# Kernel optimization log

Hardware: AMD Instinct MI355X
Metric: run time of the kernel (lower is better)

The kernel has to match this reference:

```python
import jax, jax.numpy as jnp
import numpy as np

B, T, C, HS = 8, 2048, 1024, 128


def setup_inputs() -> dict:
    key = jax.random.key(0)
    k1, k2, k3, k4 = jax.random.split(key, 4)
    return {
        "x": jax.random.normal(k1, (B, T, C), dtype=jnp.float32),
        "Wq": jax.random.normal(k2, (C, HS), dtype=jnp.float32) * (C ** -0.5),
        "Wk": jax.random.normal(k3, (C, HS), dtype=jnp.float32) * (C ** -0.5),
        "Wv": jax.random.normal(k4, (C, HS), dtype=jnp.float32) * (C ** -0.5),
    }


def _rope_tables(T, hs):
    # Matches get_rotary_embedding: d = hs//2, theta_i = 10000**(-2*(i-1)/d) for i in 0..d-1
    d = hs // 2
    i = jnp.arange(d, dtype=jnp.float32)
    theta = 10000.0 ** (-2.0 * (i - 1.0) / d)
    ang = jnp.arange(T, dtype=jnp.float32)[:, None] * theta[None, :]  # [T, d]
    return jnp.cos(ang), jnp.sin(ang)


def _rotate(t, c, s):
    # t: [B,T,hs]. Equivalent to t_m @ R_m with block-diag 2x2 rotations [[c,-s],[s,c]]:
    # out[2i] = e*c + o*s ; out[2i+1] = -e*s + o*c
    e, o = t[..., 0::2], t[..., 1::2]
    return jnp.stack([e * c + o * s, -e * s + o * c], axis=-1).reshape(t.shape)


def reference(x, Wq, Wk, Wv):
    Bx, Tx, Cx = x.shape
    hs = Wq.shape[1]
    c, s = _rope_tables(Tx, hs)
    q = _rotate(x @ Wq, c, s)  # [B,T,hs]
    k = _rotate(x @ Wk, c, s)
    v = x @ Wv
    scores = jnp.einsum("bqh,bkh->bqk", q, k) * (hs ** -0.5)  # [B,T,T]
    mask = jnp.tril(jnp.ones((Tx, Tx), dtype=bool))
    scores = jnp.where(mask, scores, -jnp.inf)
    A = jax.nn.softmax(scores, axis=-1)
    return jnp.einsum("bqk,bkh->bqh", A, v)
```

## Files before the change

### kernel.cpp

```cpp
#include <hip/hip_runtime.h>

typedef __bf16 bf16x8 __attribute__((ext_vector_type(8)));
typedef float f32x4 __attribute__((ext_vector_type(4)));

static __device__ __forceinline__ unsigned short f2bf(float f){
  unsigned int u = __builtin_bit_cast(unsigned int, f);
  u += 0x7FFFu + ((u >> 16) & 1u);
  return (unsigned short)(u >> 16);
}
static __device__ __forceinline__ float bf2f(unsigned short h){
  unsigned int u = ((unsigned int)h) << 16;
  return __builtin_bit_cast(float, u);
}

__global__ __launch_bounds__(256) void k_prepw(const float* __restrict__ Wq,
                                               const float* __restrict__ Wk,
                                               const float* __restrict__ Wv,
                                               unsigned short* __restrict__ Wtb){
  int idx = blockIdx.x * 256 + threadIdx.x;
  int m = idx >> 10;
  int k = idx & 1023;
  const float* W = (m < 128) ? Wq : ((m < 256) ? Wk : Wv);
  int n = m & 127;
  Wtb[idx] = f2bf(W[k * 128 + n]);
}

__global__ __launch_bounds__(512) void k_qkv(const float* __restrict__ x,
                                             const unsigned short* __restrict__ Wtb,
                                             unsigned short* __restrict__ Qr,
                                             unsigned short* __restrict__ Kr,
                                             unsigned short* __restrict__ Vt){
  __shared__ __align__(16) unsigned short lds[64 * 72 + 128 * 72];
  unsigned short* sA = lds;
  unsigned short* sB = lds + 64 * 72;

  int bid0 = blockIdx.x;
  int wg = (bid0 & 7) * 96 + (bid0 >> 3);
  int mblk = wg / 3;
  int nblk = wg - mblk * 3;

  int tid = threadIdx.x;
  int lane = tid & 63, wid = tid >> 6;
  int wm = wid >> 1, wn = wid & 1;
  int g = lane >> 4, lr = lane & 15;

  f32x4 acc[4] = {};
  const float* xbase = x + (size_t)(mblk * 64) * 1024;
  const unsigned short* wbase = Wtb + (size_t)(nblk * 128) * 1024;

  for (int k0 = 0; k0 < 1024; k0 += 64){
    __syncthreads();
#pragma unroll
    for (int p = 0; p < 2; p++){
      int idx = tid + p * 512;
      int r = idx >> 4, c4 = (idx & 15) * 4;
      float4 v = *reinterpret_cast<const float4*>(xbase + (size_t)r * 1024 + k0 + c4);
      uint2 pk;
      pk.x = ((unsigned int)f2bf(v.y) << 16) | f2bf(v.x);
      pk.y = ((unsigned int)f2bf(v.w) << 16) | f2bf(v.z);
      *reinterpret_cast<uint2*>(&sA[r * 72 + c4]) = pk;
    }
#pragma unroll
    for (int p = 0; p < 2; p++){
      int idx = tid + p * 512;
      int r = idx >> 3, c8 = (idx & 7) * 8;
      *reinterpret_cast<uint4*>(&sB[r * 72 + c8]) =
        *reinterpret_cast<const uint4*>(wbase + (size_t)r * 1024 + k0 + c8);
    }
    __syncthreads();

#pragma unroll
    for (int ks = 0; ks < 2; ks++){
      bf16x8 af = *reinterpret_cast<const bf16x8*>(&sA[(wm * 16 + lr) * 72 + ks * 32 + g * 8]);
      bf16x8 bfr[4];
#pragma unroll
      for (int n = 0; n < 4; n++)
        bfr[n] = *reinterpret_cast<const bf16x8*>(&sB[(wn * 64 + n * 16 + lr) * 72 + ks * 32 + g * 8]);
#pragma unroll
      for (int n = 0; n < 4; n++)
        acc[n] = __builtin_amdgcn_mfma_f32_16x16x32_bf16(af, bfr[n], acc[n], 0, 0, 0);
    }
  }
  __syncthreads();

  int row0 = mblk * 64;
  if (nblk < 2){
    unsigned short* sE = lds;
    float scale = nblk ? 1.0f : 0.12751744950370064f;
#pragma unroll
    for (int n = 0; n < 4; n++){
      int col = wn * 64 + n * 16 + lr;
      int i = col >> 1;
      float theta = exp2f(13.287712379549449f * (2.0f - 2.0f * (float)i) * 0.015625f);
      float sgn = (lr & 1) ? -1.0f : 1.0f;
#pragma unroll
      for (int r = 0; r < 4; r++){
        int tl = wm * 16 + g * 4 + r;
        int t = (row0 + tl) & 2047;
        float s, c;
        sincosf((float)t * theta, &s, &c);
        float v = acc[n][r];
        float partner = __shfl_xor(v, 1);
        float res = (v * c + partner * sgn * s) * scale;
        sE[tl * 136 + col] = f2bf(res);
      }
    }
    __syncthreads();
    unsigned short* dst = (nblk ? Kr : Qr) + (size_t)row0 * 128;
#pragma unroll
    for (int p = 0; p < 2; p++){
      int u = tid + p * 512;
      int tl = u >> 4, h0 = (u & 15) * 8;
      uint4 vv = *reinterpret_cast<const uint4*>(&sE[tl * 136 + h0]);
      *reinterpret_cast<uint4*>(dst + (size_t)tl * 128 + h0) = vv;
    }
  } else {
    unsigned short* sE = lds;
#pragma unroll
    for (int n = 0; n < 4; n++){
      int col = wn * 64 + n * 16 + lr;
#pragma unroll
      for (int r = 0; r < 4; r++){
        int tl = wm * 16 + g * 4 + r;
        sE[col * 72 + tl] = f2bf(acc[n][r]);
      }
    }
    __syncthreads();
    int b = row0 >> 11;
    int t0 = row0 & 2047;
#pragma unroll
    for (int p = 0; p < 2; p++){
      int u = tid + p * 512;
      int h = u >> 3, tc = (u & 7) * 8;
      uint4 vv = *reinterpret_cast<const uint4*>(&sE[h * 72 + tc]);
      *reinterpret_cast<uint4*>(Vt + ((size_t)(b * 128 + h)) * 2048 + t0 + tc) = vv;
    }
  }
}

__global__ __launch_bounds__(128) void k_attn_part(const unsigned short* __restrict__ Qr,
                                                   const unsigned short* __restrict__ Kr,
                                                   const unsigned short* __restrict__ Vt,
                                                   unsigned short* __restrict__ Opart,
                                                   float* __restrict__ ml){
  __shared__ __align__(16) unsigned short sK[32][136];
  __shared__ __align__(16) unsigned short sV[128][40];
  __shared__ __align__(16) unsigned short sP[2][16][40];

  int bid = blockIdx.x;
  int b = bid / 160;
  int rem = bid - b * 160;
  int qt, c;
  if (rem < 16)      { qt = rem;                    c = 0; }
  else if (rem < 48) { qt = 16 + ((rem - 16) >> 1); c = (rem - 16) & 1; }
  else if (rem < 96) { int r2 = rem - 48; int d = r2 / 3; qt = 32 + d; c = r2 - 3 * d; }
  else               { int r3 = rem - 96; qt = 48 + (r3 >> 2); c = r3 & 3; }

  int q_base = qt * 32;
  int kv_start = c * 512;
  int kv_end = min(kv_start + 512, q_base + 32);
  int niter = (kv_end - kv_start) >> 5;

  int tid = threadIdx.x, w = tid >> 6, lane = tid & 63;
  int g = lane >> 4, lr = lane & 15;

  int qrow = q_base + w * 16 + lr;
  const unsigned short* qptr = Qr + ((size_t)(b * 2048 + qrow)) * 128;
  bf16x8 qf[4];
#pragma unroll
  for (int hc = 0; hc < 4; hc++)
    qf[hc] = *reinterpret_cast<const bf16x8*>(qptr + hc * 32 + g * 8);

  f32x4 oacc[8] = {};
  float mrow = -1e30f, lrow = 0.0f;

  const unsigned short* Kb = Kr + (size_t)b * 2048 * 128;
  const unsigned short* Vb = Vt + (size_t)b * 128 * 2048;

  for (int it = 0; it < niter; it++){
    int kv0 = kv_start + it * 32;
    __syncthreads();
#pragma unroll
    for (int p = 0; p < 4; p++){
      int idx = tid + p * 128;
      int r = idx >> 4, c8 = (idx & 15) * 8;
      *reinterpret_cast<uint4*>(&sK[r][c8]) =
        *reinterpret_cast<const uint4*>(Kb + (size_t)(kv0 + r) * 128 + c8);
    }
#pragma unroll
    for (int p = 0; p < 4; p++){
      int idx = tid + p * 128;
      int h = idx >> 2, c8 = (idx & 3) * 8;
      *reinterpret_cast<uint4*>(&sV[h][c8]) =
        *reinterpret_cast<const uint4*>(Vb + (size_t)h * 2048 + kv0 + c8);
    }
    __syncthreads();

    f32x4 st[2];
#pragma unroll
    for (int ct = 0; ct < 2; ct++){
      f32x4 a = {0.f, 0.f, 0.f, 0.f};
#pragma unroll
      for (int hc = 0; hc < 4; hc++){
        bf16x8 kf = *reinterpret_cast<const bf16x8*>(&sK[ct * 16 + lr][hc * 32 + g * 8]);
        a = __builtin_amdgcn_mfma_f32_16x16x32_bf16(kf, qf[hc], a, 0, 0, 0);
      }
      st[ct] = a;
    }

    float mx = -1e30f;
#pragma unroll
    for (int ct = 0; ct < 2; ct++){
      int kvb = kv0 + ct * 16 + g * 4;
#pragma unroll
      for (int r = 0; r < 4; r++){
        float s = (kvb + r <= qrow) ? st[ct][r] : -1e30f;
        st[ct][r] = s;
        mx = fmaxf(mx, s);
      }
    }
    mx = fmaxf(mx, __shfl_xor(mx, 16));
    mx = fmaxf(mx, __shfl_xor(mx, 32));
    float m = fmaxf(mrow, mx);
    float alpha = exp2f(mrow - m);

    float rs = 0.0f;
#pragma unroll
    for (int ct = 0; ct < 2; ct++){
      float p0 = exp2f(st[ct][0] - m);
      float p1 = exp2f(st[ct][1] - m);
      float p2 = exp2f(st[ct][2] - m);
      float p3 = exp2f(st[ct][3] - m);
      rs += (p0 + p1) + (p2 + p3);
      uint2 pk;
      pk.x = ((unsigned int)f2bf(p1) << 16) | f2bf(p0);
      pk.y = ((unsigned int)f2bf(p3) << 16) | f2bf(p2);
      *reinterpret_cast<uint2*>(&sP[w][lr][ct * 16 + g * 4]) = pk;
    }
    rs += __shfl_xor(rs, 16);
    rs += __shfl_xor(rs, 32);
    lrow = lrow * alpha + rs;
    mrow = m;

    float af0 = __shfl(alpha, g * 4 + 0);
    float af1 = __shfl(alpha, g * 4 + 1);
    float af2 = __shfl(alpha, g * 4 + 2);
    float af3 = __shfl(alpha, g * 4 + 3);
#pragma unroll
    for (int ht = 0; ht < 8; ht++){
      oacc[ht][0] *= af0;
      oacc[ht][1] *= af1;
      oacc[ht][2] *= af2;
      oacc[ht][3] *= af3;
    }

    bf16x8 pa = *reinterpret_cast<const bf16x8*>(&sP[w][lr][g * 8]);
#pragma unroll
    for (int ht = 0; ht < 8; ht++){
      bf16x8 vf = *reinterpret_cast<const bf16x8*>(&sV[ht * 16 + lr][g * 8]);
      oacc[ht] = __builtin_amdgcn_mfma_f32_16x16x32_bf16(pa, vf, oacc[ht], 0, 0, 0);
    }
  }

  size_t slot = (size_t)(b * 64 + qt) * 4 + c;
  unsigned short* op = Opart + slot * 4096;
  float* mlp = ml + slot * 64;
#pragma unroll
  for (int ht = 0; ht < 8; ht++)
#pragma unroll
    for (int r = 0; r < 4; r++){
      int rowl = w * 16 + g * 4 + r;
      op[rowl * 128 + ht * 16 + lr] = f2bf(oacc[ht][r]);
    }
  if (lane < 16){
    mlp[w * 16 + lr]      = mrow;
    mlp[32 + w * 16 + lr] = lrow;
  }
}

__global__ __launch_bounds__(256) void k_comb(const unsigned short* __restrict__ Opart,
                                              const float* __restrict__ ml,
                                              float* __restrict__ out){
  int bid = blockIdx.x;
  int b = bid >> 6, qt = bid & 63;
  int nck = (qt >> 4) + 1;
  int tid = threadIdx.x;
  int row = tid >> 3;
  int col0 = (tid & 7) * 16;
  size_t slot0 = (size_t)(b * 64 + qt) * 4;

  float m_c[4], l_c[4];
  float M = -1e30f;
#pragma unroll
  for (int c = 0; c < 4; c++) if (c < nck){
    m_c[c] = ml[(slot0 + c) * 64 + row];
    l_c[c] = ml[(slot0 + c) * 64 + 32 + row];
    M = fmaxf(M, m_c[c]);
  }
  float L = 0.0f, wgt[4];
#pragma unroll
  for (int c = 0; c < 4; c++) if (c < nck){
    wgt[c] = exp2f(m_c[c] - M);
    L += wgt[c] * l_c[c];
  }
  float acc[16] = {};
#pragma unroll
  for (int c = 0; c < 4; c++) if (c < nck){
    const unsigned short* src = Opart + (slot0 + c) * 4096 + row * 128 + col0;
    uint4 u0 = *reinterpret_cast<const uint4*>(src);
    uint4 u1 = *reinterpret_cast<const uint4*>(src + 8);
    unsigned int uu[8] = {u0.x, u0.y, u0.z, u0.w, u1.x, u1.y, u1.z, u1.w};
#pragma unroll
    for (int j = 0; j < 8; j++){
      acc[2 * j]     += wgt[c] * bf2f((unsigned short)(uu[j] & 0xFFFF));
      acc[2 * j + 1] += wgt[c] * bf2f((unsigned short)(uu[j] >> 16));
    }
  }
  float invL = 1.0f / L;
  float* dst = out + ((size_t)(b * 2048 + qt * 32 + row)) * 128 + col0;
#pragma unroll
  for (int j = 0; j < 4; j++){
    float4 v = {acc[4 * j] * invL, acc[4 * j + 1] * invL,
                acc[4 * j + 2] * invL, acc[4 * j + 3] * invL};
    *reinterpret_cast<float4*>(dst + 4 * j) = v;
  }
}

extern "C" void kernel_launch(void* const* d_in, const int* in_sizes, int n_in,
                              void* d_out, int out_size, void* d_ws, size_t ws_size,
                              hipStream_t stream) {
  const float* x  = (const float*)d_in[0];
  const float* Wq = (const float*)d_in[1];
  const float* Wk = (const float*)d_in[2];
  const float* Wv = (const float*)d_in[3];
  float* out = (float*)d_out;

  char* ws = (char*)d_ws;
  unsigned short* Wtb   = (unsigned short*)ws;
  unsigned short* Qr    = (unsigned short*)(ws + 786432);
  unsigned short* Kr    = (unsigned short*)(ws + 786432 + 4194304);
  unsigned short* Vt    = (unsigned short*)(ws + 786432 + 2*4194304);
  unsigned short* Opart = (unsigned short*)(ws + 786432 + 3*4194304);
  float* ml             = (float*)(ws + 786432 + 3*4194304 + 16777216);

  hipLaunchKernelGGL(k_prepw, dim3(1536), dim3(256), 0, stream, Wq, Wk, Wv, Wtb);
  hipLaunchKernelGGL(k_qkv,   dim3(768),  dim3(512), 0, stream, x, Wtb, Qr, Kr, Vt);
  hipLaunchKernelGGL(k_attn_part, dim3(1280), dim3(128), 0, stream, Qr, Kr, Vt, Opart, ml);
  hipLaunchKernelGGL(k_comb, dim3(512), dim3(256), 0, stream, Opart, ml, out);
}
```

Baseline: 81.36 us.

## Double-buffer LDS tiles in QKV projection GEMM with register prefetch

The QKV projection kernel now prefetches the next K-slice of x and the weights into registers while MFMAs run on the current LDS buffer. It then writes that slice to a second LDS buffer, so each iteration needs one barrier instead of two. The aim is to hide global-load latency behind compute. This doubles LDS use (about 55KB per block), adds a minBlocks hint to launch_bounds, and increases register pressure.

```diff
diff --git a/kernel.cpp b/kernel.cpp
--- a/kernel.cpp
+++ b/kernel.cpp
@@ -25,14 +25,13 @@
   Wtb[idx] = f2bf(W[k * 128 + n]);
 }
 
-__global__ __launch_bounds__(512) void k_qkv(const float* __restrict__ x,
-                                             const unsigned short* __restrict__ Wtb,
-                                             unsigned short* __restrict__ Qr,
-                                             unsigned short* __restrict__ Kr,
-                                             unsigned short* __restrict__ Vt){
-  __shared__ __align__(16) unsigned short lds[64 * 72 + 128 * 72];
-  unsigned short* sA = lds;
-  unsigned short* sB = lds + 64 * 72;
+#define QKV_BUF 13824
+__global__ __launch_bounds__(512, 4) void k_qkv(const float* __restrict__ x,
+                                                const unsigned short* __restrict__ Wtb,
+                                                unsigned short* __restrict__ Qr,
+                                                unsigned short* __restrict__ Kr,
+                                                unsigned short* __restrict__ Vt){
+  __shared__ __align__(16) unsigned short lds[2 * QKV_BUF];
 
   int bid0 = blockIdx.x;
   int wg = (bid0 & 7) * 96 + (bid0 >> 3);
@@ -48,37 +47,71 @@
   const float* xbase = x + (size_t)(mblk * 64) * 1024;
   const unsigned short* wbase = Wtb + (size_t)(nblk * 128) * 1024;
 
-  for (int k0 = 0; k0 < 1024; k0 += 64){
-    __syncthreads();
-#pragma unroll
-    for (int p = 0; p < 2; p++){
-      int idx = tid + p * 512;
-      int r = idx >> 4, c4 = (idx & 15) * 4;
-      float4 v = *reinterpret_cast<const float4*>(xbase + (size_t)r * 1024 + k0 + c4);
+  int ra0 = tid >> 4,          ca0 = (tid & 15) * 4;
+  int ra1 = (tid + 512) >> 4,  ca1 = (tid & 15) * 4;
+  int rb0 = tid >> 3,          cb0 = (tid & 7) * 8;
+  int rb1 = (tid + 512) >> 3,  cb1 = (tid & 7) * 8;
+
+  float4 fa0, fa1; uint4 ub0, ub1;
+  fa0 = *reinterpret_cast<const float4*>(xbase + (size_t)ra0 * 1024 + ca0);
+  fa1 = *reinterpret_cast<const float4*>(xbase + (size_t)ra1 * 1024 + ca1);
+  ub0 = *reinterpret_cast<const uint4*>(wbase + (size_t)rb0 * 1024 + cb0);
+  ub1 = *reinterpret_cast<const uint4*>(wbase + (size_t)rb1 * 1024 + cb1);
+  {
+    unsigned short* sA = lds;
+    unsigned short* sB = lds + 64 * 72;
+    uint2 pk;
+    pk.x = ((unsigned int)f2bf(fa0.y) << 16) | f2bf(fa0.x);
+    pk.y = ((unsigned int)f2bf(fa0.w) << 16) | f2bf(fa0.z);
+    *reinterpret_cast<uint2*>(&sA[ra0 * 72 + ca0]) = pk;
+    pk.x = ((unsigned int)f2bf(fa1.y) << 16) | f2bf(fa1.x);
+    pk.y = ((unsigned int)f2bf(fa1.w) << 16) | f2bf(fa1.z);
+    *reinterpret_cast<uint2*>(&sA[ra1 * 72 + ca1]) = pk;
+    *reinterpret_cast<uint4*>(&sB[rb0 * 72 + cb0]) = ub0;
+    *reinterpret_cast<uint4*>(&sB[rb1 * 72 + cb1]) = ub1;
+  }
+  __syncthreads();
+
+  int cur = 0;
+  for (int t = 0; t < 16; t++){
+    if (t < 15){
+      int k0n = (t + 1) * 64;
+      fa0 = *reinterpret_cast<const float4*>(xbase + (size_t)ra0 * 1024 + k0n + ca0);
+      fa1 = *reinterpret_cast<const float4*>(xbase + (size_t)ra1 * 1024 + k0n + ca1);
+      ub0 = *reinterpret_cast<const uint4*>(wbase + (size_t)rb0 * 1024 + k0n + cb0);
+      ub1 = *reinterpret_cast<const uint4*>(wbase + (size_t)rb1 * 1024 + k0n + cb1);
+    }
+
+    {
+      const unsigned short* sA = lds + cur * QKV_BUF;
+      const unsigned short* sB = sA + 64 * 72;
+#pragma unroll
+      for (int ks = 0; ks < 2; ks++){
+        bf16x8 af = *reinterpret_cast<const bf16x8*>(&sA[(wm * 16 + lr) * 72 + ks * 32 + g * 8]);
+        bf16x8 bfr[4];
+#pragma unroll
+        for (int n = 0; n < 4; n++)
+          bfr[n] = *reinterpret_cast<const bf16x8*>(&sB[(wn * 64 + n * 16 + lr) * 72 + ks * 32 + g * 8]);
+#pragma unroll
+        for (int n = 0; n < 4; n++)
+          acc[n] = __builtin_amdgcn_mfma_f32_16x16x32_bf16(af, bfr[n], acc[n], 0, 0, 0);
+      }
+    }
+
+    if (t < 15){
+      unsigned short* sA = lds + (cur ^ 1) * QKV_BUF;
+      unsigned short* sB = sA + 64 * 72;
       uint2 pk;
-      pk.x = ((unsigned int)f2bf(v.y) << 16) | f2bf(v.x);
-      pk.y = ((unsigned int)f2bf(v.w) << 16) | f2bf(v.z);
-      *reinterpret_cast<uint2*>(&sA[r * 72 + c4]) = pk;
-    }
-#pragma unroll
-    for (int p = 0; p < 2; p++){
-      int idx = tid + p * 512;
-      int r = idx >> 3, c8 = (idx & 7) * 8;
-      *reinterpret_cast<uint4*>(&sB[r * 72 + c8]) =
-        *reinterpret_cast<const uint4*>(wbase + (size_t)r * 1024 + k0 + c8);
-    }
-    __syncthreads();
-
-#pragma unroll
-    for (int ks = 0; ks < 2; ks++){
-      bf16x8 af = *reinterpret_cast<const bf16x8*>(&sA[(wm * 16 + lr) * 72 + ks * 32 + g * 8]);
-      bf16x8 bfr[4];
-#pragma unroll
-      for (int n = 0; n < 4; n++)
-        bfr[n] = *reinterpret_cast<const bf16x8*>(&sB[(wn * 64 + n * 16 + lr) * 72 + ks * 32 + g * 8]);
-#pragma unroll
-      for (int n = 0; n < 4; n++)
-        acc[n] = __builtin_amdgcn_mfma_f32_16x16x32_bf16(af, bfr[n], acc[n], 0, 0, 0);
+      pk.x = ((unsigned int)f2bf(fa0.y) << 16) | f2bf(fa0.x);
+      pk.y = ((unsigned int)f2bf(fa0.w) << 16) | f2bf(fa0.z);
+      *reinterpret_cast<uint2*>(&sA[ra0 * 72 + ca0]) = pk;
+      pk.x = ((unsigned int)f2bf(fa1.y) << 16) | f2bf(fa1.x);
+      pk.y = ((unsigned int)f2bf(fa1.w) << 16) | f2bf(fa1.z);
+      *reinterpret_cast<uint2*>(&sA[ra1 * 72 + ca1]) = pk;
+      *reinterpret_cast<uint4*>(&sB[rb0 * 72 + cb0]) = ub0;
+      *reinterpret_cast<uint4*>(&sB[rb1 * 72 + cb1]) = ub1;
+      __syncthreads();
+      cur ^= 1;
     }
   }
   __syncthreads();
```

New measurement: 85.60 us. 1.05x slower.

## Use direct global-to-LDS loads with XOR swizzle in QKV projection GEMM

Applied to the files above, without the earlier changes.

The QKV projection kernel now loads the bf16 weight tiles straight into LDS with global_load_lds, skipping the register round-trip. The LDS layout changes from padded rows of 72 elements to unpadded 64-element rows with an XOR swizzle, which avoids bank conflicts and shrinks LDS use. The x tile is now loaded as 8 floats per thread and converted with the native bf16 cast, which replaces the manual rounding routine. This kernel is only the projection part of the whole attention pipeline, so any effect on total time is limited.

```diff
diff --git a/kernel.cpp b/kernel.cpp
--- a/kernel.cpp
+++ b/kernel.cpp
@@ -3,10 +3,12 @@
 typedef __bf16 bf16x8 __attribute__((ext_vector_type(8)));
 typedef float f32x4 __attribute__((ext_vector_type(4)));
 
+typedef const unsigned int __attribute__((address_space(1)))* gptr_t;
+typedef unsigned int __attribute__((address_space(3)))* lptr_t;
+
 static __device__ __forceinline__ unsigned short f2bf(float f){
-  unsigned int u = __builtin_bit_cast(unsigned int, f);
-  u += 0x7FFFu + ((u >> 16) & 1u);
-  return (unsigned short)(u >> 16);
+  __bf16 h = (__bf16)f;
+  return __builtin_bit_cast(unsigned short, h);
 }
 static __device__ __forceinline__ float bf2f(unsigned short h){
   unsigned int u = ((unsigned int)h) << 16;
@@ -30,9 +32,10 @@
                                              unsigned short* __restrict__ Qr,
                                              unsigned short* __restrict__ Kr,
                                              unsigned short* __restrict__ Vt){
-  __shared__ __align__(16) unsigned short lds[64 * 72 + 128 * 72];
+  __shared__ __align__(16) unsigned short lds[64 * 64 + 128 * 64];
+
   unsigned short* sA = lds;
-  unsigned short* sB = lds + 64 * 72;
+  unsigned short* sB = lds + 64 * 64;
 
   int bid0 = blockIdx.x;
   int wg = (bid0 & 7) * 96 + (bid0 >> 3);
@@ -48,37 +51,46 @@
   const float* xbase = x + (size_t)(mblk * 64) * 1024;
   const unsigned short* wbase = Wtb + (size_t)(nblk * 128) * 1024;
 
-  for (int k0 = 0; k0 < 1024; k0 += 64){
-    __syncthreads();
-#pragma unroll
-    for (int p = 0; p < 2; p++){
-      int idx = tid + p * 512;
-      int r = idx >> 4, c4 = (idx & 15) * 4;
-      float4 v = *reinterpret_cast<const float4*>(xbase + (size_t)r * 1024 + k0 + c4);
-      uint2 pk;
-      pk.x = ((unsigned int)f2bf(v.y) << 16) | f2bf(v.x);
-      pk.y = ((unsigned int)f2bf(v.w) << 16) | f2bf(v.z);
-      *reinterpret_cast<uint2*>(&sA[r * 72 + c4]) = pk;
-    }
-#pragma unroll
-    for (int p = 0; p < 2; p++){
-      int idx = tid + p * 512;
-      int r = idx >> 3, c8 = (idx & 7) * 8;
-      *reinterpret_cast<uint4*>(&sB[r * 72 + c8]) =
-        *reinterpret_cast<const uint4*>(wbase + (size_t)r * 1024 + k0 + c8);
-    }
-    __syncthreads();
-
+  int ar = tid >> 3, ac = tid & 7;
+  const float* agp = xbase + (size_t)ar * 1024 + ac * 8;
+  char* awp = (char*)sA + ar * 128 + (((ac ^ (ar & 7))) << 4);
+  int bp = tid & 7;
+  int br1 = tid >> 3, br2 = br1 + 64;
+  const unsigned short* bgp1 = wbase + (size_t)br1 * 1024 + ((bp ^ (br1 & 7)) << 3);
+  const unsigned short* bgp2 = wbase + (size_t)br2 * 1024 + ((bp ^ (br2 & 7)) << 3);
+  unsigned short* bdst1 = sB + wid * 512;
+  unsigned short* bdst2 = sB + 4096 + wid * 512;
+
+  for (int t = 0; t < 16; t++){
+    int k0 = t * 64;
+    if (t) __syncthreads();
+    __builtin_amdgcn_global_load_lds((gptr_t)(const void*)(bgp1 + k0),
+                                     (lptr_t)(void*)bdst1, 16, 0, 0);
+    __builtin_amdgcn_global_load_lds((gptr_t)(const void*)(bgp2 + k0),
+                                     (lptr_t)(void*)bdst2, 16, 0, 0);
+    float4 v0 = *reinterpret_cast<const float4*>(agp + k0);
+    float4 v1 = *reinterpret_cast<const float4*>(agp + k0 + 4);
+    union { bf16x8 h; uint4 u4; } pk;
+    pk.h[0] = (__bf16)v0.x; pk.h[1] = (__bf16)v0.y;
+    pk.h[2] = (__bf16)v0.z; pk.h[3] = (__bf16)v0.w;
+    pk.h[4] = (__bf16)v1.x; pk.h[5] = (__bf16)v1.y;
+    pk.h[6] = (__bf16)v1.z; pk.h[7] = (__bf16)v1.w;
+    *reinterpret_cast<uint4*>(awp) = pk.u4;
+    __syncthreads();
+
+    int arow = wm * 16 + lr;
+    int asw = (arow & 7) << 4;
 #pragma unroll
     for (int ks = 0; ks < 2; ks++){
-      bf16x8 af = *reinterpret_cast<const bf16x8*>(&sA[(wm * 16 + lr) * 72 + ks * 32 + g * 8]);
-      bf16x8 bfr[4];
-#pragma unroll
-      for (int n = 0; n < 4; n++)
-        bfr[n] = *reinterpret_cast<const bf16x8*>(&sB[(wn * 64 + n * 16 + lr) * 72 + ks * 32 + g * 8]);
-#pragma unroll
-      for (int n = 0; n < 4; n++)
-        acc[n] = __builtin_amdgcn_mfma_f32_16x16x32_bf16(af, bfr[n], acc[n], 0, 0, 0);
+      bf16x8 af = *reinterpret_cast<const bf16x8*>(
+          (const char*)sA + arow * 128 + ((ks * 64 + g * 16) ^ asw));
+#pragma unroll
+      for (int n = 0; n < 4; n++){
+        int brow = wn * 64 + n * 16 + lr;
+        bf16x8 bn = *reinterpret_cast<const bf16x8*>(
+            (const char*)sB + brow * 128 + ((ks * 64 + g * 16) ^ ((brow & 7) << 4)));
+        acc[n] = __builtin_amdgcn_mfma_f32_16x16x32_bf16(af, bn, acc[n], 0, 0, 0);
+      }
     }
   }
   __syncthreads();
```

New measurement: 77.39 us. -4.9%, faster.
